# Kernel optimization log

Measured on AMD Instinct MI355X. Metric: run time of the kernel, lower is better.

## Reference

```python
import jax, jax.numpy as jnp
import numpy as np

MUL = 256            # multiplicity of each irrep block
S = MUL              # scalar (0e) block width
V = MUL * 3          # vector (1e) block width
D = S + V            # total feature width = 1024
N = 32768            # number of nodes
INV3 = 1.0 / np.sqrt(3.0)   # w3j(1,1,0) and w3j(0,1,1) coefficient
INV6 = 1.0 / np.sqrt(6.0)   # w3j(1,1,1) (Levi-Civita) coefficient
A0 = np.sqrt(1.0 / 5.0)     # path weight for 0e outputs: sqrt(dim_out / n_paths) = sqrt(1/5)
A1 = np.sqrt(3.0 / 5.0)     # path weight for 1e outputs: sqrt(3/5)


def _split(x):
    # x: [N, D] -> scalars [N, MUL], vectors [N, MUL, 3]
    return x[:, :S], x[:, S:].reshape(x.shape[0], MUL, 3)


def norm_gate(x, w1, b1, w2, b2):
    # NormGate: gates = MLP([scalars, |vectors|]); out = [gates_s, vectors * gates_v]
    s, v = _split(x)
    nv = jnp.sqrt(jnp.sum(v * v, axis=-1) + 1e-12)           # [N, MUL] per-irrep norms
    f0 = jnp.concatenate([s, nv], axis=-1)                    # [N, 2*MUL]
    g = jax.nn.silu(f0 @ w1 + b1) @ w2 + b2                   # [N, 2*MUL]
    gated = v * g[:, S:, None]                                # ElementwiseTensorProduct with 0e gates
    return jnp.concatenate([g[:, :S], gated.reshape(-1, V)], axis=-1)


def irrep_linear(x, w0, b0, w1):
    # e3nn o3.Linear: per-l multiplicity mixing with 1/sqrt(fan_in) normalization; bias only on 0e
    s, v = _split(x)
    so = s @ (w0 / np.sqrt(MUL)) + b0
    vo = jnp.einsum('nui,uw->nwi', v, w1 / np.sqrt(MUL))
    return jnp.concatenate([so, vo.reshape(-1, V)], axis=-1)


def tensor_product(x1, x2, w):
    # 'uuu' CG tensor product, 5 instructions: (0,0)->0, (0,1)->1, (1,0)->1, (1,1)->0, (1,1)->1
    # w: [5, MUL] per-path per-u learned weights
    s1, v1 = _split(x1)
    s2, v2 = _split(x2)
    out0 = A0 * (w[0] * s1 * s2 + w[3] * INV3 * jnp.sum(v1 * v2, axis=-1))   # [N, MUL]
    out1 = A1 * (INV3 * (w[1] * s1)[:, :, None] * v2
                 + INV3 * (w[2] * s2)[:, :, None] * v1
                 + INV6 * w[4][None, :, None] * jnp.cross(v1, v2))           # [N, MUL, 3]
    return jnp.concatenate([out0, out1.reshape(-1, V)], axis=-1)


def setup_inputs() -> dict:
    key = jax.random.key(0)
    ks = jax.random.split(key, 32)
    d = {}
    d['x'] = jax.random.normal(ks[0], (N, D), dtype=jnp.float32)
    d['old_fii'] = jax.random.normal(ks[1], (N, D), dtype=jnp.float32)
    i = 2
    for pre in ('ng1', 'ng2', 'ngo'):
        d[pre + '_w1'] = jax.random.normal(ks[i], (2 * MUL, 2 * MUL), dtype=jnp.float32) / np.sqrt(2 * MUL); i += 1
        d[pre + '_b1'] = jax.random.normal(ks[i], (2 * MUL,), dtype=jnp.float32) * 0.01; i += 1
        d[pre + '_w2'] = jax.random.normal(ks[i], (2 * MUL, 2 * MUL), dtype=jnp.float32) / np.sqrt(2 * MUL); i += 1
        d[pre + '_b2'] = jax.random.normal(ks[i], (2 * MUL,), dtype=jnp.float32) * 0.01; i += 1
    for pre in ('lin1', 'lin2', 'lin3'):
        d[pre + '_w0'] = jax.random.normal(ks[i], (MUL, MUL), dtype=jnp.float32); i += 1
        d[pre + '_b0'] = jax.random.normal(ks[i], (MUL,), dtype=jnp.float32) * 0.01; i += 1
        d[pre + '_w1'] = jax.random.normal(ks[i], (MUL, MUL), dtype=jnp.float32); i += 1
    d['tp_w'] = jax.random.normal(ks[i], (5, MUL), dtype=jnp.float32)
    return d


def reference(x, old_fii,
              ng1_w1, ng1_b1, ng1_w2, ng1_b2,
              ng2_w1, ng2_b1, ng2_w2, ng2_b2,
              ngo_w1, ngo_b1, ngo_w2, ngo_b2,
              lin1_w0, lin1_b0, lin1_w1,
              lin2_w0, lin2_b0, lin2_w1,
              lin3_w0, lin3_b0, lin3_w1,
              tp_w):
    xl = irrep_linear(norm_gate(x, ng1_w1, ng1_b1, ng1_w2, ng1_b2), lin1_w0, lin1_b0, lin1_w1)
    xr = irrep_linear(norm_gate(x, ng2_w1, ng2_b1, ng2_w2, ng2_b2), lin2_w0, lin2_b0, lin2_w1)
    t = tensor_product(xl, xr, tp_w) + x        # resnet (dims match)
    t = irrep_linear(norm_gate(t, ngo_w1, ngo_b1, ngo_w2, ngo_b2), lin3_w0, lin3_b0, lin3_w1)
    return old_fii + t
```

## Files before the change

kernel.cpp:

```cpp
#include <hip/hip_runtime.h>
#include <stdint.h>
#include <math.h>

typedef unsigned short u16;
typedef __attribute__((ext_vector_type(8))) short short8;
typedef __attribute__((ext_vector_type(4))) float f32x4;

#define A0C 0.44721359549995793f
#define A1C 0.77459666924148340f
#define INV3C 0.57735026918962584f
#define INV6C 0.40824829046386302f

__device__ __forceinline__ float bf2f(u16 u) {
    unsigned v = ((unsigned)u) << 16; float f; __builtin_memcpy(&f, &v, 4); return f;
}
__device__ __forceinline__ u16 f2bf(float f) {
    unsigned u; __builtin_memcpy(&u, &f, 4);
    u += 0x7fffu + ((u >> 16) & 1u);
    return (u16)(u >> 16);
}

__device__ __forceinline__ void gload_lds16(const void* g, void* l) {
    __builtin_amdgcn_global_load_lds((const __attribute__((address_space(1))) unsigned*)g,
                                     (__attribute__((address_space(3))) unsigned*)l, 16, 0, 0);
}

struct WDesc { const float* s; u16* d; int n; float sc; };
struct WArgs { WDesc w[12]; };

__global__ void cvt_weights(WArgs args) {
    WDesc wd = args.w[blockIdx.z];
    int n = wd.n;
    int x0 = blockIdx.x * 32, y0 = blockIdx.y * 32;
    if (x0 >= n || y0 >= n) return;
    __shared__ float tile[32][33];
    int tx = threadIdx.x, ty = threadIdx.y;
#pragma unroll
    for (int j = 0; j < 4; j++)
        tile[ty + 8 * j][tx] = wd.s[(size_t)(y0 + ty + 8 * j) * n + x0 + tx];
    __syncthreads();
#pragma unroll
    for (int j = 0; j < 4; j++)
        wd.d[(size_t)(x0 + ty + 8 * j) * n + y0 + tx] = f2bf(tile[tx][ty + 8 * j] * wd.sc);
}

struct BDesc { const float* s; float* d; int n; };
struct BArgs { BDesc b[9]; };
__global__ void pack_bias(BArgs a) {
    BDesc b = a.b[blockIdx.x];
    for (int i = threadIdx.x; i < b.n; i += 256) b.d[i] = b.s[i];
}

__global__ void prep_f0(const float* __restrict__ x, u16* __restrict__ f0,
                        u16* __restrict__ xv, long ps) {
    __shared__ float row[1024];
    int n = blockIdx.x, u = threadIdx.x;
    const float4* xr = (const float4*)(x + (size_t)n * 1024);
    float4 v4 = xr[u];
    row[4 * u] = v4.x; row[4 * u + 1] = v4.y; row[4 * u + 2] = v4.z; row[4 * u + 3] = v4.w;
    __syncthreads();
    float s = row[u];
    float v0 = row[256 + 3 * u], v1 = row[256 + 3 * u + 1], v2 = row[256 + 3 * u + 2];
    float nv = sqrtf(v0 * v0 + v1 * v1 + v2 * v2 + 1e-12f);
    size_t o = (size_t)n * 256 + u;
    f0[(size_t)n * 512 + u] = f2bf(s);
    f0[(size_t)n * 512 + 256 + u] = f2bf(nv);
    xv[o] = f2bf(v0);
    xv[ps + o] = f2bf(v1);
    xv[2 * ps + o] = f2bf(v2);
}

__global__ __launch_bounds__(512, 2)
void gemm256(const u16* __restrict__ Ap, int lda, long az,
             const u16* __restrict__ xsrc,
             const u16* __restrict__ gp, int gld, long gz,
             const u16* __restrict__ Bt, long bz, long bw,
             const float* __restrict__ bias, int bsz,
             u16* __restrict__ C, int ldc, long czs, long czp,
             int K, long nc, int mode, int act, int nshift)
{
    extern __shared__ __align__(16) u16 sm[];
    u16* As = sm;
    u16* Bs = sm + 32768;

    const int tid = threadIdx.x;
    const int lane = tid & 63;
    const int wid = tid >> 6;
    const int wr = wid >> 2, wc = wid & 3;
    const int lr = lane & 15, hk = lane >> 4;

    int nwg = gridDim.x;
    int lid = blockIdx.x;
    int wg;
    if ((nwg & 7) == 0) { int q = nwg >> 3; wg = (lid & 7) * q + (lid >> 3); }
    else wg = lid;
    const long row0 = (long)(wg >> nshift) * 256;
    const int n0 = (wg & ((1 << nshift) - 1)) * 256;
    const int zi = blockIdx.y;

    long p = 0, rr0 = row0;
    if (mode == 2) { p = row0 / nc; rr0 = row0 - p * nc; }

    const u16* Bz = Bt + (size_t)zi * bz + ((mode == 2 && p > 0) ? bw : 0);
    const long cbase = (mode == 2) ? (zi * czs + p * czp + rr0 * ldc)
                                   : (zi * czs + row0 * ldc);

    f32x4 acc[8][4];
#pragma unroll
    for (int m = 0; m < 8; m++)
#pragma unroll
        for (int n = 0; n < 4; n++) acc[m][n] = (f32x4){0.f, 0.f, 0.f, 0.f};

    auto stageB = [&](int buf, int kt) {
#pragma unroll
        for (int it = 0; it < 4; ++it) {
            int idx = it * 512 + tid;
            int r = idx >> 3, s = idx & 7;
            const u16* g = Bz + (size_t)(n0 + r) * K + kt + ((s ^ (r & 7)) * 8);
            u16* l = Bs + buf * 16384 + (size_t)(it * 512 + (tid & 0x1C0)) * 8;
            gload_lds16(g, l);
        }
    };
    auto stageA0 = [&](int buf, int kt) {
#pragma unroll
        for (int it = 0; it < 4; ++it) {
            int idx = it * 512 + tid;
            int r = idx >> 3, s = idx & 7;
            const u16* g = Ap + (size_t)zi * az + (rr0 + r) * (size_t)lda + kt + ((s ^ (r & 7)) * 8);
            u16* l = As + buf * 16384 + (size_t)(it * 512 + (tid & 0x1C0)) * 8;
            gload_lds16(g, l);
        }
    };
    auto stageA2 = [&](int buf, int kt) {
#pragma unroll
        for (int it = 0; it < 4; ++it) {
            int idx = it * 512 + tid;
            int r = idx >> 3, s = idx & 7;
            int u = kt + s * 8;
            union { short8 v; u16 h[8]; } gg, tu, pk;
            gg.v = *(const short8*)(gp + (size_t)zi * gz + (rr0 + r) * (size_t)gld + 256 + u);
            tu.v = *(const short8*)(xsrc + (size_t)(row0 - nc + r) * 256 + u);
#pragma unroll
            for (int j = 0; j < 8; j++) pk.h[j] = f2bf(bf2f(tu.h[j]) * bf2f(gg.h[j]));
            *(short8*)&As[buf * 16384 + ((size_t)r * 8 + (s ^ (r & 7))) * 8] = pk.v;
        }
    };

    const bool a_direct = (mode == 0) || (p == 0);
    const int nt = K >> 6;
    stageB(0, 0);
    if (a_direct) stageA0(0, 0); else stageA2(0, 0);
    __syncthreads();

    int buf = 0;
    for (int t = 0; t < nt; ++t) {
        if (t + 1 < nt) {
            int kt = (t + 1) << 6;
            stageB(buf ^ 1, kt);
            if (a_direct) stageA0(buf ^ 1, kt); else stageA2(buf ^ 1, kt);
        }
        const int ao = buf * 16384, bo = buf * 16384;
#pragma unroll
        for (int kk = 0; kk < 2; ++kk) {
            short8 b[4];
#pragma unroll
            for (int n = 0; n < 4; n++) {
                int cb = wc * 64 + n * 16 + lr;
                int sl = (kk * 4 + hk) ^ (cb & 7);
                b[n] = *(const short8*)&Bs[bo + (size_t)cb * 64 + sl * 8];
            }
#pragma unroll
            for (int m = 0; m < 8; m++) {
                int ra = wr * 128 + m * 16 + lr;
                int sl = (kk * 4 + hk) ^ (ra & 7);
                short8 a = *(const short8*)&As[ao + (size_t)ra * 64 + sl * 8];
#pragma unroll
                for (int n = 0; n < 4; n++)
                    acc[m][n] = __builtin_amdgcn_mfma_f32_16x16x32_bf16(a, b[n], acc[m][n], 0, 0, 0);
            }
        }
        __syncthreads();
        buf ^= 1;
    }

    const bool use_bias = bias && (mode == 0 || p == 0);
#pragma unroll
    for (int n = 0; n < 4; n++) {
        int col = n0 + wc * 64 + n * 16 + lr;
        float bv = use_bias ? bias[(size_t)zi * bsz + col] : 0.0f;
#pragma unroll
        for (int m = 0; m < 8; m++) {
#pragma unroll
            for (int j = 0; j < 4; j++) {
                long rit = wr * 128 + m * 16 + hk * 4 + j;
                float v = acc[m][n][j] + bv;
                if (act) v = v * (1.0f / (1.0f + __expf(-v)));
                C[cbase + rit * (size_t)ldc + col] = f2bf(v);
            }
        }
    }
}

__global__ void tp_res(const u16* __restrict__ xl, const u16* xr_,
                       const float* __restrict__ tpw, const u16* __restrict__ xv,
                       u16* f0, u16* tv, long ps)
{
    int n = blockIdx.x, u = threadIdx.x;
    size_t o = (size_t)n * 256 + u;
    float s1 = bf2f(xl[o]);
    float a1x = bf2f(xl[ps + o]), a1y = bf2f(xl[2 * ps + o]), a1z = bf2f(xl[3 * ps + o]);
    float s2 = bf2f(xr_[o]);
    float b1x = bf2f(xr_[ps + o]), b1y = bf2f(xr_[2 * ps + o]), b1z = bf2f(xr_[3 * ps + o]);
    float xs = bf2f(f0[(size_t)n * 512 + u]);
    float rx = bf2f(xv[o]), ry = bf2f(xv[ps + o]), rz = bf2f(xv[2 * ps + o]);
    float w0 = tpw[u], w1 = tpw[256 + u], w2 = tpw[512 + u], w3 = tpw[768 + u], w4 = tpw[1024 + u];

    float dot = a1x * b1x + a1y * b1y + a1z * b1z;
    float cx = a1y * b1z - a1z * b1y;
    float cy = a1z * b1x - a1x * b1z;
    float cz = a1x * b1y - a1y * b1x;

    float out0 = A0C * (w0 * s1 * s2 + w3 * INV3C * dot) + xs;
    float ox = A1C * (INV3C * (w1 * s1 * b1x + w2 * s2 * a1x) + INV6C * w4 * cx) + rx;
    float oy = A1C * (INV3C * (w1 * s1 * b1y + w2 * s2 * a1y) + INV6C * w4 * cy) + ry;
    float oz = A1C * (INV3C * (w1 * s1 * b1z + w2 * s2 * a1z) + INV6C * w4 * cz) + rz;

    float nv = sqrtf(ox * ox + oy * oy + oz * oz + 1e-12f);
    f0[(size_t)n * 512 + u] = f2bf(out0);
    f0[(size_t)n * 512 + 256 + u] = f2bf(nv);
    tv[o] = f2bf(ox);
    tv[ps + o] = f2bf(oy);
    tv[2 * ps + o] = f2bf(oz);
}

__global__ void repack(const u16* __restrict__ outp, const float* __restrict__ old,
                       float* __restrict__ out, long ps)
{
    __shared__ float add[1024];
    int n = blockIdx.x, u = threadIdx.x;
    size_t o = (size_t)n * 256 + u;
    add[u] = bf2f(outp[o]);
    float vx = bf2f(outp[ps + o]);
    float vy = bf2f(outp[2 * ps + o]);
    float vz = bf2f(outp[3 * ps + o]);
    add[256 + 3 * u] = vx;
    add[256 + 3 * u + 1] = vy;
    add[256 + 3 * u + 2] = vz;
    __syncthreads();
    float4 o4 = ((const float4*)(old + (size_t)n * 1024))[u];
    float4 r;
    r.x = o4.x + add[4 * u];
    r.y = o4.y + add[4 * u + 1];
    r.z = o4.z + add[4 * u + 2];
    r.w = o4.w + add[4 * u + 3];
    ((float4*)(out + (size_t)n * 1024))[u] = r;
}

enum {
    OFF_ng12w1 = 0,
    OFF_ng1w2  = 524288,
    OFF_ngow1  = 1048576,
    OFF_ngow2  = 1310720,
    OFF_l12w0  = 1572864,
    OFF_l12w1  = 1703936,
    OFF_l3w0   = 1835008,
    OFF_l3w1   = 1900544
};
#define BIAS_BYTE_OFF 3932160
enum { BOFF_mlp1 = 0, BOFF_mlp2 = 1024, BOFF_ngo1 = 2048, BOFF_ngo2 = 2560,
       BOFF_l12 = 3072, BOFF_l3 = 3584 };

extern "C" void kernel_launch(void* const* d_in, const int* in_sizes, int n_in,
                              void* d_out, int out_size, void* d_ws, size_t ws_size,
                              hipStream_t stream) {
    const float* x      = (const float*)d_in[0];
    const float* oldf   = (const float*)d_in[1];
    const float* ng1_w1 = (const float*)d_in[2];
    const float* ng1_b1 = (const float*)d_in[3];
    const float* ng1_w2 = (const float*)d_in[4];
    const float* ng1_b2 = (const float*)d_in[5];
    const float* ng2_w1 = (const float*)d_in[6];
    const float* ng2_b1 = (const float*)d_in[7];
    const float* ng2_w2 = (const float*)d_in[8];
    const float* ng2_b2 = (const float*)d_in[9];
    const float* ngo_w1 = (const float*)d_in[10];
    const float* ngo_b1 = (const float*)d_in[11];
    const float* ngo_w2 = (const float*)d_in[12];
    const float* ngo_b2 = (const float*)d_in[13];
    const float* l1_w0  = (const float*)d_in[14];
    const float* l1_b0  = (const float*)d_in[15];
    const float* l1_w1  = (const float*)d_in[16];
    const float* l2_w0  = (const float*)d_in[17];
    const float* l2_b0  = (const float*)d_in[18];
    const float* l2_w1  = (const float*)d_in[19];
    const float* l3_w0  = (const float*)d_in[20];
    const float* l3_b0  = (const float*)d_in[21];
    const float* l3_w1  = (const float*)d_in[22];
    const float* tpw    = (const float*)d_in[23];

    u16* wts = (u16*)d_ws;
    char* wsb = (char*)d_ws;
    float* biasf = (float*)(wsb + BIAS_BYTE_OFF);

    WArgs wa;
    wa.w[0]  = { ng1_w1, wts + OFF_ng12w1,          512, 1.0f };
    wa.w[1]  = { ng2_w1, wts + OFF_ng12w1 + 262144, 512, 1.0f };
    wa.w[2]  = { ng1_w2, wts + OFF_ng1w2,           512, 1.0f };
    wa.w[3]  = { ng2_w2, wts + OFF_ng1w2 + 262144,  512, 1.0f };
    wa.w[4]  = { ngo_w1, wts + OFF_ngow1,           512, 1.0f };
    wa.w[5]  = { ngo_w2, wts + OFF_ngow2,           512, 1.0f };
    wa.w[6]  = { l1_w0, wts + OFF_l12w0,            256, 0.0625f };
    wa.w[7]  = { l2_w0, wts + OFF_l12w0 + 65536,    256, 0.0625f };
    wa.w[8]  = { l1_w1, wts + OFF_l12w1,            256, 0.0625f };
    wa.w[9]  = { l2_w1, wts + OFF_l12w1 + 65536,    256, 0.0625f };
    wa.w[10] = { l3_w0, wts + OFF_l3w0,             256, 0.0625f };
    wa.w[11] = { l3_w1, wts + OFF_l3w1,             256, 0.0625f };
    cvt_weights<<<dim3(16, 16, 12), dim3(32, 8), 0, stream>>>(wa);

    BArgs ba;
    ba.b[0] = { ng1_b1, biasf + BOFF_mlp1,       512 };
    ba.b[1] = { ng2_b1, biasf + BOFF_mlp1 + 512, 512 };
    ba.b[2] = { ng1_b2, biasf + BOFF_mlp2,       512 };
    ba.b[3] = { ng2_b2, biasf + BOFF_mlp2 + 512, 512 };
    ba.b[4] = { ngo_b1, biasf + BOFF_ngo1,       512 };
    ba.b[5] = { ngo_b2, biasf + BOFF_ngo2,       512 };
    ba.b[6] = { l1_b0, biasf + BOFF_l12,         256 };
    ba.b[7] = { l2_b0, biasf + BOFF_l12 + 256,   256 };
    ba.b[8] = { l3_b0, biasf + BOFF_l3,          256 };
    pack_bias<<<9, 256, 0, stream>>>(ba);

    long Nn = (long)in_sizes[0] / 1024;

    int c = 1;
    while (c < 256 &&
           (unsigned long long)(4ULL << 20) + (unsigned long long)(Nn / c) * 10752ULL > (unsigned long long)ws_size)
        c <<= 1;
    long Nc = Nn / c;

    u16* F0 = (u16*)(wsb + (4 << 20));
    u16* H  = F0 + (size_t)Nc * 512;
    u16* G  = H + (size_t)Nc * 1024;
    u16* XV = G + (size_t)Nc * 1024;
    u16* XL = XV + (size_t)Nc * 768;
    long ps = Nc * 256;
    u16* XR = XL + 4 * ps;
    u16* TV = XR + ps;
    u16* OUTP = XL;

    dim3 blk(512);
    const size_t SMEM = 131072;
    int mt = (int)(Nc / 256);

    for (int ch = 0; ch < c; ++ch) {
        const float* xk  = x + (size_t)ch * Nc * 1024;
        const float* ok  = oldf + (size_t)ch * Nc * 1024;
        float* outk = (float*)d_out + (size_t)ch * Nc * 1024;

        prep_f0<<<(int)Nc, 256, 0, stream>>>(xk, F0, XV, ps);

        gemm256<<<dim3(mt * 4, 1), blk, SMEM, stream>>>(F0, 512, 0, nullptr, nullptr, 0, 0,
            wts + OFF_ng12w1, 0, 0, biasf + BOFF_mlp1, 0, H, 1024, 0, 0, 512, Nc, 0, 1, 2);
        gemm256<<<dim3(mt * 2, 2), blk, SMEM, stream>>>(H, 1024, 512, nullptr, nullptr, 0, 0,
            wts + OFF_ng1w2, 262144, 0, biasf + BOFF_mlp2, 512, G, 1024, 512, 0, 512, Nc, 0, 0, 1);
        gemm256<<<dim3(mt * 4, 2), blk, SMEM, stream>>>(G, 1024, 512, XV, G, 1024, 512,
            wts + OFF_l12w0, 65536, 131072, biasf + BOFF_l12, 256, XL, 256, 4 * ps, ps, 256, Nc, 2, 0, 0);

        tp_res<<<(int)Nc, 256, 0, stream>>>(XL, XR, tpw, XV, F0, TV, ps);

        gemm256<<<dim3(mt * 2, 1), blk, SMEM, stream>>>(F0, 512, 0, nullptr, nullptr, 0, 0,
            wts + OFF_ngow1, 0, 0, biasf + BOFF_ngo1, 0, H, 512, 0, 0, 512, Nc, 0, 1, 1);
        gemm256<<<dim3(mt * 2, 1), blk, SMEM, stream>>>(H, 512, 0, nullptr, nullptr, 0, 0,
            wts + OFF_ngow2, 0, 0, biasf + BOFF_ngo2, 0, G, 512, 0, 0, 512, Nc, 0, 0, 1);
        gemm256<<<dim3(mt * 4, 1), blk, SMEM, stream>>>(G, 512, 0, TV, G, 512, 0,
            wts + OFF_l3w0, 0, 65536, biasf + BOFF_l3, 0, OUTP, 256, 0, ps, 256, Nc, 2, 0, 0);

        repack<<<(int)Nc, 256, 0, stream>>>(OUTP, ok, outk, ps);
    }
}
```

Before: 539.2 us.

## Vectorize elementwise kernels and transpose MFMA operands for packed GEMM epilogue stores

The elementwise kernels (prep_f0, tp_res, repack) now have each thread handle 8 consecutive channels. They use 16-byte bf16 loads and stores and float4 accesses, with no LDS staging or block barriers, and the grid shrinks to Nc/8 blocks. In the GEMM the MFMA operands are swapped, so each lane's 4 accumulator values lie along columns instead of rows. That lets the epilogue load a float4 of bias and write four bf16 outputs as one 8-byte store instead of scattered 2-byte stores. This targets uncoalesced narrow memory traffic in the epilogue and the bandwidth-bound elementwise passes. The cost is higher register use per thread and strided 96-byte vector reads and writes per thread in the vector parts.

```diff
diff --git a/kernel.cpp b/kernel.cpp
--- a/kernel.cpp
+++ b/kernel.cpp
@@ -24,6 +24,8 @@
     __builtin_amdgcn_global_load_lds((const __attribute__((address_space(1))) unsigned*)g,
                                      (__attribute__((address_space(3))) unsigned*)l, 16, 0, 0);
 }
+
+union S8 { short8 v; u16 h[8]; };
 
 struct WDesc { const float* s; u16* d; int n; float sc; };
 struct WArgs { WDesc w[12]; };
@@ -53,21 +55,34 @@
 
 __global__ void prep_f0(const float* __restrict__ x, u16* __restrict__ f0,
                         u16* __restrict__ xv, long ps) {
-    __shared__ float row[1024];
-    int n = blockIdx.x, u = threadIdx.x;
-    const float4* xr = (const float4*)(x + (size_t)n * 1024);
-    float4 v4 = xr[u];
-    row[4 * u] = v4.x; row[4 * u + 1] = v4.y; row[4 * u + 2] = v4.z; row[4 * u + 3] = v4.w;
-    __syncthreads();
-    float s = row[u];
-    float v0 = row[256 + 3 * u], v1 = row[256 + 3 * u + 1], v2 = row[256 + 3 * u + 2];
-    float nv = sqrtf(v0 * v0 + v1 * v1 + v2 * v2 + 1e-12f);
-    size_t o = (size_t)n * 256 + u;
-    f0[(size_t)n * 512 + u] = f2bf(s);
-    f0[(size_t)n * 512 + 256 + u] = f2bf(nv);
-    xv[o] = f2bf(v0);
-    xv[ps + o] = f2bf(v1);
-    xv[2 * ps + o] = f2bf(v2);
+    int t = blockIdx.x * 256 + threadIdx.x;
+    long n = t >> 5;
+    int u0 = (t & 31) * 8;
+    const float* xr = x + (size_t)n * 1024;
+    float4 s0 = *(const float4*)(xr + u0);
+    float4 s1 = *(const float4*)(xr + u0 + 4);
+    float vv[24];
+#pragma unroll
+    for (int i = 0; i < 6; i++) {
+        float4 w = *(const float4*)(xr + 256 + 3 * u0 + 4 * i);
+        vv[4 * i] = w.x; vv[4 * i + 1] = w.y; vv[4 * i + 2] = w.z; vv[4 * i + 3] = w.w;
+    }
+    float sc[8] = { s0.x, s0.y, s0.z, s0.w, s1.x, s1.y, s1.z, s1.w };
+    S8 fs, fn, px, py, pz;
+#pragma unroll
+    for (int j = 0; j < 8; j++) {
+        float a = vv[3 * j], b = vv[3 * j + 1], c = vv[3 * j + 2];
+        float nv = sqrtf(a * a + b * b + c * c + 1e-12f);
+        fs.h[j] = f2bf(sc[j]);
+        fn.h[j] = f2bf(nv);
+        px.h[j] = f2bf(a); py.h[j] = f2bf(b); pz.h[j] = f2bf(c);
+    }
+    size_t o = (size_t)n * 256 + u0;
+    *(short8*)(f0 + (size_t)n * 512 + u0) = fs.v;
+    *(short8*)(f0 + (size_t)n * 512 + 256 + u0) = fn.v;
+    *(short8*)(xv + o) = px.v;
+    *(short8*)(xv + ps + o) = py.v;
+    *(short8*)(xv + 2 * ps + o) = pz.v;
 }
 
 __global__ __launch_bounds__(512, 2)
@@ -137,7 +152,7 @@
             int idx = it * 512 + tid;
             int r = idx >> 3, s = idx & 7;
             int u = kt + s * 8;
-            union { short8 v; u16 h[8]; } gg, tu, pk;
+            S8 gg, tu, pk;
             gg.v = *(const short8*)(gp + (size_t)zi * gz + (rr0 + r) * (size_t)gld + 256 + u);
             tu.v = *(const short8*)(xsrc + (size_t)(row0 - nc + r) * 256 + u);
 #pragma unroll
@@ -176,7 +191,7 @@
                 short8 a = *(const short8*)&As[ao + (size_t)ra * 64 + sl * 8];
 #pragma unroll
                 for (int n = 0; n < 4; n++)
-                    acc[m][n] = __builtin_amdgcn_mfma_f32_16x16x32_bf16(a, b[n], acc[m][n], 0, 0, 0);
+                    acc[m][n] = __builtin_amdgcn_mfma_f32_16x16x32_bf16(b[n], a, acc[m][n], 0, 0, 0);
             }
         }
         __syncthreads();
@@ -185,18 +200,28 @@
 
     const bool use_bias = bias && (mode == 0 || p == 0);
 #pragma unroll
-    for (int n = 0; n < 4; n++) {
-        int col = n0 + wc * 64 + n * 16 + lr;
-        float bv = use_bias ? bias[(size_t)zi * bsz + col] : 0.0f;
-#pragma unroll
-        for (int m = 0; m < 8; m++) {
-#pragma unroll
-            for (int j = 0; j < 4; j++) {
-                long rit = wr * 128 + m * 16 + hk * 4 + j;
-                float v = acc[m][n][j] + bv;
-                if (act) v = v * (1.0f / (1.0f + __expf(-v)));
-                C[cbase + rit * (size_t)ldc + col] = f2bf(v);
+    for (int m = 0; m < 8; m++) {
+        long rit = wr * 128 + m * 16 + lr;
+        u16* crow = C + cbase + rit * (size_t)ldc;
+#pragma unroll
+        for (int n = 0; n < 4; n++) {
+            int col = n0 + wc * 64 + n * 16 + hk * 4;
+            float4 bb = use_bias ? *(const float4*)&bias[(size_t)zi * bsz + col]
+                                 : (float4){0.f, 0.f, 0.f, 0.f};
+            float v0 = acc[m][n][0] + bb.x;
+            float v1 = acc[m][n][1] + bb.y;
+            float v2 = acc[m][n][2] + bb.z;
+            float v3 = acc[m][n][3] + bb.w;
+            if (act) {
+                v0 = v0 * (1.0f / (1.0f + __expf(-v0)));
+                v1 = v1 * (1.0f / (1.0f + __expf(-v1)));
+                v2 = v2 * (1.0f / (1.0f + __expf(-v2)));
+                v3 = v3 * (1.0f / (1.0f + __expf(-v3)));
             }
+            uint2 st;
+            st.x = (unsigned)f2bf(v0) | ((unsigned)f2bf(v1) << 16);
+            st.y = (unsigned)f2bf(v2) | ((unsigned)f2bf(v3) << 16);
+            *(uint2*)(crow + col) = st;
         }
     }
 }
@@ -205,55 +230,103 @@
                        const float* __restrict__ tpw, const u16* __restrict__ xv,
                        u16* f0, u16* tv, long ps)
 {
-    int n = blockIdx.x, u = threadIdx.x;
-    size_t o = (size_t)n * 256 + u;
-    float s1 = bf2f(xl[o]);
-    float a1x = bf2f(xl[ps + o]), a1y = bf2f(xl[2 * ps + o]), a1z = bf2f(xl[3 * ps + o]);
-    float s2 = bf2f(xr_[o]);
-    float b1x = bf2f(xr_[ps + o]), b1y = bf2f(xr_[2 * ps + o]), b1z = bf2f(xr_[3 * ps + o]);
-    float xs = bf2f(f0[(size_t)n * 512 + u]);
-    float rx = bf2f(xv[o]), ry = bf2f(xv[ps + o]), rz = bf2f(xv[2 * ps + o]);
-    float w0 = tpw[u], w1 = tpw[256 + u], w2 = tpw[512 + u], w3 = tpw[768 + u], w4 = tpw[1024 + u];
-
-    float dot = a1x * b1x + a1y * b1y + a1z * b1z;
-    float cx = a1y * b1z - a1z * b1y;
-    float cy = a1z * b1x - a1x * b1z;
-    float cz = a1x * b1y - a1y * b1x;
-
-    float out0 = A0C * (w0 * s1 * s2 + w3 * INV3C * dot) + xs;
-    float ox = A1C * (INV3C * (w1 * s1 * b1x + w2 * s2 * a1x) + INV6C * w4 * cx) + rx;
-    float oy = A1C * (INV3C * (w1 * s1 * b1y + w2 * s2 * a1y) + INV6C * w4 * cy) + ry;
-    float oz = A1C * (INV3C * (w1 * s1 * b1z + w2 * s2 * a1z) + INV6C * w4 * cz) + rz;
-
-    float nv = sqrtf(ox * ox + oy * oy + oz * oz + 1e-12f);
-    f0[(size_t)n * 512 + u] = f2bf(out0);
-    f0[(size_t)n * 512 + 256 + u] = f2bf(nv);
-    tv[o] = f2bf(ox);
-    tv[ps + o] = f2bf(oy);
-    tv[2 * ps + o] = f2bf(oz);
+    int t = blockIdx.x * 256 + threadIdx.x;
+    long n = t >> 5;
+    int u0 = (t & 31) * 8;
+    size_t o = (size_t)n * 256 + u0;
+
+    S8 S1, AX, AY, AZ, S2, BX, BY, BZ, XS, RX, RY, RZ;
+    S1.v = *(const short8*)(xl + o);
+    AX.v = *(const short8*)(xl + ps + o);
+    AY.v = *(const short8*)(xl + 2 * ps + o);
+    AZ.v = *(const short8*)(xl + 3 * ps + o);
+    S2.v = *(const short8*)(xr_ + o);
+    BX.v = *(const short8*)(xr_ + ps + o);
+    BY.v = *(const short8*)(xr_ + 2 * ps + o);
+    BZ.v = *(const short8*)(xr_ + 3 * ps + o);
+    XS.v = *(const short8*)(f0 + (size_t)n * 512 + u0);
+    RX.v = *(const short8*)(xv + o);
+    RY.v = *(const short8*)(xv + ps + o);
+    RZ.v = *(const short8*)(xv + 2 * ps + o);
+
+    float W[5][8];
+#pragma unroll
+    for (int q = 0; q < 5; q++) {
+        float4 a = *(const float4*)(tpw + q * 256 + u0);
+        float4 b = *(const float4*)(tpw + q * 256 + u0 + 4);
+        W[q][0] = a.x; W[q][1] = a.y; W[q][2] = a.z; W[q][3] = a.w;
+        W[q][4] = b.x; W[q][5] = b.y; W[q][6] = b.z; W[q][7] = b.w;
+    }
+
+    S8 O0, NV, TX, TY, TZ;
+#pragma unroll
+    for (int j = 0; j < 8; j++) {
+        float s1 = bf2f(S1.h[j]), a1x = bf2f(AX.h[j]), a1y = bf2f(AY.h[j]), a1z = bf2f(AZ.h[j]);
+        float s2 = bf2f(S2.h[j]), b1x = bf2f(BX.h[j]), b1y = bf2f(BY.h[j]), b1z = bf2f(BZ.h[j]);
+        float dot = a1x * b1x + a1y * b1y + a1z * b1z;
+        float cx = a1y * b1z - a1z * b1y;
+        float cy = a1z * b1x - a1x * b1z;
+        float cz = a1x * b1y - a1y * b1x;
+        float out0 = A0C * (W[0][j] * s1 * s2 + W[3][j] * INV3C * dot) + bf2f(XS.h[j]);
+        float ox = A1C * (INV3C * (W[1][j] * s1 * b1x + W[2][j] * s2 * a1x) + INV6C * W[4][j] * cx) + bf2f(RX.h[j]);
+        float oy = A1C * (INV3C * (W[1][j] * s1 * b1y + W[2][j] * s2 * a1y) + INV6C * W[4][j] * cy) + bf2f(RY.h[j]);
+        float oz = A1C * (INV3C * (W[1][j] * s1 * b1z + W[2][j] * s2 * a1z) + INV6C * W[4][j] * cz) + bf2f(RZ.h[j]);
+        float nv = sqrtf(ox * ox + oy * oy + oz * oz + 1e-12f);
+        O0.h[j] = f2bf(out0);
+        NV.h[j] = f2bf(nv);
+        TX.h[j] = f2bf(ox); TY.h[j] = f2bf(oy); TZ.h[j] = f2bf(oz);
+    }
+    *(short8*)(f0 + (size_t)n * 512 + u0) = O0.v;
+    *(short8*)(f0 + (size_t)n * 512 + 256 + u0) = NV.v;
+    *(short8*)(tv + o) = TX.v;
+    *(short8*)(tv + ps + o) = TY.v;
+    *(short8*)(tv + 2 * ps + o) = TZ.v;
 }
 
 __global__ void repack(const u16* __restrict__ outp, const float* __restrict__ old,
                        float* __restrict__ out, long ps)
 {
-    __shared__ float add[1024];
-    int n = blockIdx.x, u = threadIdx.x;
-    size_t o = (size_t)n * 256 + u;
-    add[u] = bf2f(outp[o]);
-    float vx = bf2f(outp[ps + o]);
-    float vy = bf2f(outp[2 * ps + o]);
-    float vz = bf2f(outp[3 * ps + o]);
-    add[256 + 3 * u] = vx;
-    add[256 + 3 * u + 1] = vy;
-    add[256 + 3 * u + 2] = vz;
-    __syncthreads();
-    float4 o4 = ((const float4*)(old + (size_t)n * 1024))[u];
-    float4 r;
-    r.x = o4.x + add[4 * u];
-    r.y = o4.y + add[4 * u + 1];
-    r.z = o4.z + add[4 * u + 2];
-    r.w = o4.w + add[4 * u + 3];
-    ((float4*)(out + (size_t)n * 1024))[u] = r;
+    int t = blockIdx.x * 256 + threadIdx.x;
+    long n = t >> 5;
+    int u0 = (t & 31) * 8;
+    size_t o = (size_t)n * 256 + u0;
+
+    S8 S, VX, VY, VZ;
+    S.v  = *(const short8*)(outp + o);
+    VX.v = *(const short8*)(outp + ps + o);
+    VY.v = *(const short8*)(outp + 2 * ps + o);
+    VZ.v = *(const short8*)(outp + 3 * ps + o);
+
+    const float* oldr = old + (size_t)n * 1024;
+    float* outr = out + (size_t)n * 1024;
+
+#pragma unroll
+    for (int i = 0; i < 2; i++) {
+        float4 ov = *(const float4*)(oldr + u0 + 4 * i);
+        float4 r;
+        r.x = ov.x + bf2f(S.h[4 * i]);
+        r.y = ov.y + bf2f(S.h[4 * i + 1]);
+        r.z = ov.z + bf2f(S.h[4 * i + 2]);
+        r.w = ov.w + bf2f(S.h[4 * i + 3]);
+        *(float4*)(outr + u0 + 4 * i) = r;
+    }
+    float vv[24];
+#pragma unroll
+    for (int j = 0; j < 8; j++) {
+        vv[3 * j] = bf2f(VX.h[j]);
+        vv[3 * j + 1] = bf2f(VY.h[j]);
+        vv[3 * j + 2] = bf2f(VZ.h[j]);
+    }
+#pragma unroll
+    for (int i = 0; i < 6; i++) {
+        float4 ov = *(const float4*)(oldr + 256 + 3 * u0 + 4 * i);
+        float4 r;
+        r.x = ov.x + vv[4 * i];
+        r.y = ov.y + vv[4 * i + 1];
+        r.z = ov.z + vv[4 * i + 2];
+        r.w = ov.w + vv[4 * i + 3];
+        *(float4*)(outr + 256 + 3 * u0 + 4 * i) = r;
+    }
 }
 
 enum {
@@ -350,13 +423,14 @@
     dim3 blk(512);
     const size_t SMEM = 131072;
     int mt = (int)(Nc / 256);
+    int eb = (int)(Nc / 8);
 
     for (int ch = 0; ch < c; ++ch) {
         const float* xk  = x + (size_t)ch * Nc * 1024;
         const float* ok  = oldf + (size_t)ch * Nc * 1024;
         float* outk = (float*)d_out + (size_t)ch * Nc * 1024;
 
-        prep_f0<<<(int)Nc, 256, 0, stream>>>(xk, F0, XV, ps);
+        prep_f0<<<eb, 256, 0, stream>>>(xk, F0, XV, ps);
 
         gemm256<<<dim3(mt * 4, 1), blk, SMEM, stream>>>(F0, 512, 0, nullptr, nullptr, 0, 0,
             wts + OFF_ng12w1, 0, 0, biasf + BOFF_mlp1, 0, H, 1024, 0, 0, 512, Nc, 0, 1, 2);
@@ -365,7 +439,7 @@
         gemm256<<<dim3(mt * 4, 2), blk, SMEM, stream>>>(G, 1024, 512, XV, G, 1024, 512,
             wts + OFF_l12w0, 65536, 131072, biasf + BOFF_l12, 256, XL, 256, 4 * ps, ps, 256, Nc, 2, 0, 0);
 
-        tp_res<<<(int)Nc, 256, 0, stream>>>(XL, XR, tpw, XV, F0, TV, ps);
+        tp_res<<<eb, 256, 0, stream>>>(XL, XR, tpw, XV, F0, TV, ps);
 
         gemm256<<<dim3(mt * 2, 1), blk, SMEM, stream>>>(F0, 512, 0, nullptr, nullptr, 0, 0,
             wts + OFF_ngow1, 0, 0, biasf + BOFF_ngo1, 0, H, 512, 0, 0, 512, Nc, 0, 1, 1);
@@ -374,6 +448,6 @@
         gemm256<<<dim3(mt * 4, 1), blk, SMEM, stream>>>(G, 512, 0, TV, G, 512, 0,
             wts + OFF_l3w0, 0, 65536, biasf + BOFF_l3, 0, OUTP, 256, 0, ps, 256, Nc, 2, 0, 0);
 
-        repack<<<(int)Nc, 256, 0, stream>>>(OUTP, ok, outk, ps);
-    }
-}
+        repack<<<eb, 256, 0, stream>>>(OUTP, ok, outk, ps);
+    }
+}
```

Measured after the change: 504.3 us. 1.07x faster.
